# Kernel tuning notes

Measured on AMD Instinct MI355X. Metric: run time of the kernel, lower is better.

The kernel has to match this reference:

```python
import jax, jax.numpy as jnp
import numpy as np

# Poincare ball, curvature c = 1.0 (manifold.c)
C = 1.0
SQC = 1.0  # sqrt(C)
EPS = 1e-15
BALL_EPS = 1e-5
ALPHA = 0.1  # params[0]


def _project(x):
    # clip points back inside the open ball
    norm = jnp.linalg.norm(x, axis=-1, keepdims=True)
    maxnorm = (1.0 - BALL_EPS) / SQC
    return jnp.where(norm > maxnorm, x / jnp.maximum(norm, EPS) * maxnorm, x)


def _artanh(x):
    return jnp.arctanh(jnp.clip(x, -1.0 + 1e-7, 1.0 - 1e-7))


def _lambda_x(x):
    # conformal factor lambda_x = 2 / (1 - c||x||^2)
    return 2.0 / jnp.maximum(1.0 - C * jnp.sum(x * x, axis=-1, keepdims=True), EPS)


def _mobius_scalar_mul(r, x):
    n = jnp.maximum(jnp.linalg.norm(x, axis=-1, keepdims=True), EPS)
    return jnp.tanh(r * _artanh(SQC * n)) * x / (SQC * n)


def _mobius_add(x, y):
    x2 = jnp.sum(x * x, axis=-1, keepdims=True)
    y2 = jnp.sum(y * y, axis=-1, keepdims=True)
    xy = jnp.sum(x * y, axis=-1, keepdims=True)
    num = (1.0 + 2.0 * C * xy + C * y2) * x + (1.0 - C * x2) * y
    den = 1.0 + 2.0 * C * xy + C * C * x2 * y2
    return num / jnp.maximum(den, EPS)


def _expmap0(u):
    n = jnp.maximum(jnp.linalg.norm(u, axis=-1, keepdims=True), EPS)
    return jnp.tanh(SQC * n) * u / (SQC * n)


def _mobius_matvec(W, x):
    # Mobius matrix-vector multiply: expmap0-style rescale of x @ W^T
    xn = jnp.maximum(jnp.linalg.norm(x, axis=-1, keepdims=True), EPS)
    mx = x @ W.T
    mxn = jnp.maximum(jnp.linalg.norm(mx, axis=-1, keepdims=True), EPS)
    res = jnp.tanh(mxn / xn * _artanh(SQC * xn)) * mx / (SQC * mxn)
    return _project(res)


def _clamp_abs(x, eps=1e-10):
    return jnp.where(x >= 0, jnp.maximum(x, eps), jnp.minimum(x, -eps))


def weighted_midpoint_spmm(x, src, dst, w, n):
    # gyro-midpoint of neighbors under sparse adjacency weights
    gamma = _lambda_x(x)                                   # [N,1]
    msg = (gamma * x)[src] * w[:, None]                    # [E,d] irregular gather
    num = jax.ops.segment_sum(msg, dst, num_segments=n)    # [N,d]
    den = jax.ops.segment_sum(jnp.abs(w) * (gamma[:, 0] - 1.0)[src], dst,
                              num_segments=n)[:, None]     # [N,1]
    return _project(_mobius_scalar_mul(0.5, num / _clamp_abs(den)))


def weighted_midpoint_pair(a, b, wa, wb):
    # weighted_midpoint(stack([a,b],dim=1), weights=[wa,wb], reducedim=[1])
    ga, gb = _lambda_x(a), _lambda_x(b)
    num = wa * ga * a + wb * gb * b
    den = abs(wa) * (ga - 1.0) + abs(wb) * (gb - 1.0)
    return _project(_mobius_scalar_mul(0.5, num / _clamp_abs(den)))


def setup_inputs() -> dict:
    key = jax.random.key(0)
    kx, kh, kw, kW, kb, ks, kd = jax.random.split(key, 7)
    N, D, E = 100000, 48, 1600000

    def to_ball(u):
        # squash gaussian samples well inside the Poincare ball
        n = jnp.linalg.norm(u, axis=-1, keepdims=True)
        return 0.5 * u / (1.0 + n)

    x = to_ball(jax.random.normal(kx, (N, D), dtype=jnp.float32))
    h_init = to_ball(jax.random.normal(kh, (N, D), dtype=jnp.float32))
    edge_w = jax.random.uniform(kw, (E,), dtype=jnp.float32, minval=0.01, maxval=1.0)
    W = jax.random.normal(kW, (D, D), dtype=jnp.float32) * (1.0 / np.sqrt(D))
    bias = jax.random.normal(kb, (D,), dtype=jnp.float32) * 0.01
    edge_src = jax.random.randint(ks, (E,), 0, N, dtype=jnp.int32)
    edge_dst = jax.random.randint(kd, (E,), 0, N, dtype=jnp.int32)
    return {"x": x, "h_init": h_init, "edge_w": edge_w, "W": W, "bias": bias,
            "edge_src": edge_src, "edge_dst": edge_dst}


def reference(x, h_init, edge_w, W, bias, edge_src, edge_dst):
    n = x.shape[0]
    # 1) sparse adjacency-weighted hyperbolic midpoint aggregation
    support = weighted_midpoint_spmm(x, edge_src, edge_dst, edge_w, n)
    # 2) residual midpoint with h_init, weights [1-alpha, alpha]
    support = weighted_midpoint_pair(support, h_init, 1.0 - ALPHA, ALPHA)
    # 3) Mobius linear (HyperbolicLinearFast, eval-mode dropout, no nonlin)
    h = _mobius_matvec(W, support)
    h = _project(_mobius_add(h, _expmap0(bias[None, :])))
    return h
```

## Files before the change

kernel.cpp:

```cpp
#include <hip/hip_runtime.h>
#include <math.h>

#define D  48
#define DQ 12
#define SPAN 128
#define SHIFT 7
#define PCH  8192
#define PTH  512

constexpr float F_EPS   = 1e-15f;
constexpr float MAXNORM = 1.0f - 1e-5f;

__device__ __forceinline__ float artanh_c(float x) {
    x = fminf(x, 1.0f - 1e-7f);
    x = fmaxf(x, -1.0f + 1e-7f);
    return atanhf(x);
}

__device__ __forceinline__ float clampabs(float x) {
    return (x >= 0.0f) ? fmaxf(x, 1e-10f) : fminf(x, -1e-10f);
}

__device__ __forceinline__ unsigned short f2bf(float f) {
    unsigned u = __float_as_uint(f);
    u += 0x7FFFu + ((u >> 16) & 1u);
    return (unsigned short)(u >> 16);
}

__device__ __forceinline__ float bf2f(unsigned short u) {
    return __uint_as_float(((unsigned)u) << 16);
}

__global__ void k_gamma(const float* __restrict__ x, float* __restrict__ gam,
                        int* __restrict__ ghist, int n, int nb)
{
    int i = blockIdx.x * blockDim.x + threadIdx.x;
    if (i < nb) ghist[i] = 0;
    if (i >= n) return;
    const float4* xr = reinterpret_cast<const float4*>(x) + (size_t)i * DQ;
    float s = 0.0f;
#pragma unroll
    for (int q = 0; q < DQ; ++q) {
        float4 v = xr[q];
        s += v.x * v.x + v.y * v.y + v.z * v.z + v.w * v.w;
    }
    gam[i] = 2.0f / fmaxf(1.0f - s, F_EPS);
}

__global__ __launch_bounds__(PTH) void k_hist(const int* __restrict__ dst,
                                              int* __restrict__ ghist, int E, int nb)
{
    __shared__ int h[1024];
    int t = threadIdx.x;
    for (int i = t; i < 1024; i += PTH) h[i] = 0;
    __syncthreads();
    int base = blockIdx.x * PCH;
#pragma unroll 4
    for (int k = 0; k < PCH / PTH; ++k) {
        int i = base + k * PTH + t;
        if (i < E) {
            unsigned b = ((unsigned)dst[i]) >> SHIFT;
            if (b < 1024u) atomicAdd(&h[b], 1);
        }
    }
    __syncthreads();
    for (int i = t; i < nb; i += PTH) {
        int c = h[i];
        if (c) atomicAdd(&ghist[i], c);
    }
}

__global__ __launch_bounds__(1024) void k_scanb(const int* __restrict__ ghist,
                                                int* __restrict__ gstart,
                                                int* __restrict__ gcur, int nb, int E)
{
    __shared__ int sh[1024];
    int t = threadIdx.x;
    int v = (t < nb) ? ghist[t] : 0;
    sh[t] = v;
    __syncthreads();
    for (int off = 1; off < 1024; off <<= 1) {
        int a = sh[t];
        int b = (t >= off) ? sh[t - off] : 0;
        __syncthreads();
        sh[t] = a + b;
        __syncthreads();
    }
    if (t < nb) { int s = sh[t] - v; gstart[t] = s; gcur[t] = s; }
    if (t == 0) gstart[nb] = E;
}

__global__ __launch_bounds__(PTH) void k_part(const int* __restrict__ src,
                                              const int* __restrict__ dst,
                                              const float* __restrict__ w,
                                              const float* __restrict__ gam,
                                              int* __restrict__ gcur,
                                              int2* __restrict__ seg, int E, int nb)
{
    __shared__ int hist[1024];
    __shared__ int base_[1024];
    __shared__ int lcur[1024];
    int t = threadIdx.x;
    for (int i = t; i < 1024; i += PTH) { hist[i] = 0; base_[i] = 0; lcur[i] = 0; }
    __syncthreads();
    int b0 = blockIdx.x * PCH;
#pragma unroll 4
    for (int k = 0; k < PCH / PTH; ++k) {
        int i = b0 + k * PTH + t;
        if (i < E) {
            unsigned b = ((unsigned)dst[i]) >> SHIFT;
            if (b < 1024u) atomicAdd(&hist[b], 1);
        }
    }
    __syncthreads();
    for (int i = t; i < nb; i += PTH) {
        int c = hist[i];
        if (c) base_[i] = atomicAdd(&gcur[i], c);
    }
    __syncthreads();
#pragma unroll 4
    for (int k = 0; k < PCH / PTH; ++k) {
        int i = b0 + k * PTH + t;
        if (i < E) {
            int d = dst[i];
            unsigned b = ((unsigned)d) >> SHIFT;
            if (b < 1024u) {
                int s = src[i];
                float wv = w[i];
                float g  = gam[s];
                unsigned short wb  = f2bf(wv);
                unsigned short wdb = f2bf(fabsf(wv) * (g - 1.0f));
                int pos = base_[b] + atomicAdd(&lcur[b], 1);
                if (pos >= 0 && pos < E) {
                    int2 r;
                    r.x = ((d & (SPAN - 1)) << 24) | (s & 0xFFFFFF);
                    r.y = ((unsigned)wb << 16) | wdb;
                    seg[pos] = r;
                }
            }
        }
    }
}

__global__ __launch_bounds__(256) void k_sortb(
    const int2* __restrict__ seg, const int* __restrict__ gstart,
    int* __restrict__ starts, int2* __restrict__ seg2, int n, int E)
{
    __shared__ int hist[SPAN];
    __shared__ int sb[SPAN];
    __shared__ int cur[SPAN];
    int b = blockIdx.x;
    int t = threadIdx.x;
    if (b == 0 && t == 0) starts[n] = E;
    int segL = gstart[b], segR = gstart[b + 1];
    if (segL < 0) segL = 0;
    if (segR > E) segR = E;
    if (t < SPAN) hist[t] = 0;
    __syncthreads();
    {
        int j = segL + t;
        for (; j + 768 < segR; j += 1024) {
            unsigned d0 = ((unsigned)seg[j      ].x) >> 24;
            unsigned d1 = ((unsigned)seg[j + 256].x) >> 24;
            unsigned d2 = ((unsigned)seg[j + 512].x) >> 24;
            unsigned d3 = ((unsigned)seg[j + 768].x) >> 24;
            atomicAdd(&hist[d0], 1);
            atomicAdd(&hist[d1], 1);
            atomicAdd(&hist[d2], 1);
            atomicAdd(&hist[d3], 1);
        }
        for (; j < segR; j += 256) {
            unsigned dl = ((unsigned)seg[j].x) >> 24;
            atomicAdd(&hist[dl], 1);
        }
    }
    __syncthreads();
    if (t < SPAN) sb[t] = hist[t];
    __syncthreads();
    for (int off = 1; off < SPAN; off <<= 1) {
        int a = 0;
        if (t < SPAN) { a = sb[t]; if (t >= off) a += sb[t - off]; }
        __syncthreads();
        if (t < SPAN) sb[t] = a;
        __syncthreads();
    }
    if (t < SPAN) {
        int ls = sb[t] - hist[t];
        cur[t] = segL + ls;
        int node = b * SPAN + t;
        if (node < n) starts[node] = segL + ls;
    }
    __syncthreads();
    {
        int j = segL + t;
        for (; j + 768 < segR; j += 1024) {
            int2 r0 = seg[j      ];
            int2 r1 = seg[j + 256];
            int2 r2 = seg[j + 512];
            int2 r3 = seg[j + 768];
            int p0 = atomicAdd(&cur[((unsigned)r0.x) >> 24], 1);
            int p1 = atomicAdd(&cur[((unsigned)r1.x) >> 24], 1);
            int p2 = atomicAdd(&cur[((unsigned)r2.x) >> 24], 1);
            int p3 = atomicAdd(&cur[((unsigned)r3.x) >> 24], 1);
            if (p0 >= 0 && p0 < E) seg2[p0] = make_int2(r0.x & 0xFFFFFF, r0.y);
            if (p1 >= 0 && p1 < E) seg2[p1] = make_int2(r1.x & 0xFFFFFF, r1.y);
            if (p2 >= 0 && p2 < E) seg2[p2] = make_int2(r2.x & 0xFFFFFF, r2.y);
            if (p3 >= 0 && p3 < E) seg2[p3] = make_int2(r3.x & 0xFFFFFF, r3.y);
        }
        for (; j < segR; j += 256) {
            int2 r = seg[j];
            int pos = atomicAdd(&cur[((unsigned)r.x) >> 24], 1);
            if (pos >= 0 && pos < E) seg2[pos] = make_int2(r.x & 0xFFFFFF, r.y);
        }
    }
}

__global__ __launch_bounds__(256) void k_prep(const float* __restrict__ x,
                                              const float* __restrict__ gam,
                                              ushort4* __restrict__ ybf, int n)
{
    long long t = (long long)blockIdx.x * blockDim.x + threadIdx.x;
    int node = (int)(t / DQ);
    if (node >= n) return;
    int part = (int)(t % DQ);
    float g = gam[node];
    float4 v = reinterpret_cast<const float4*>(x)[(size_t)node * DQ + part];
    ushort4 o;
    o.x = f2bf(v.x * g);
    o.y = f2bf(v.y * g);
    o.z = f2bf(v.z * g);
    o.w = f2bf(v.w * g);
    ybf[(size_t)node * DQ + part] = o;
}

__global__ __launch_bounds__(256) void k_gather(
    const ushort4* __restrict__ ybf,
    const int* __restrict__ starts,
    const int2* __restrict__ srec,
    float* __restrict__ num, float* __restrict__ den, int n, int E)
{
    long long t = (long long)blockIdx.x * blockDim.x + threadIdx.x;
    int node = (int)(t / DQ);
    if (node >= n) return;
    int part = (int)(t % DQ);
    int j0 = starts[node], j1 = starts[node + 1];
    if (j0 < 0) j0 = 0;
    if (j1 > E) j1 = E;
    float4 acc = make_float4(0.f, 0.f, 0.f, 0.f);
    float dacc = 0.f;
    int j = j0;
    for (; j + 3 < j1; j += 4) {
        int2 r0 = srec[j];
        int2 r1 = srec[j + 1];
        int2 r2 = srec[j + 2];
        int2 r3 = srec[j + 3];
        ushort4 a0 = ybf[(size_t)(r0.x) * DQ + part];
        ushort4 a1 = ybf[(size_t)(r1.x) * DQ + part];
        ushort4 a2 = ybf[(size_t)(r2.x) * DQ + part];
        ushort4 a3 = ybf[(size_t)(r3.x) * DQ + part];
        float w0 = bf2f((unsigned short)(((unsigned)r0.y) >> 16));
        float w1 = bf2f((unsigned short)(((unsigned)r1.y) >> 16));
        float w2 = bf2f((unsigned short)(((unsigned)r2.y) >> 16));
        float w3 = bf2f((unsigned short)(((unsigned)r3.y) >> 16));
        acc.x = fmaf(w0, bf2f(a0.x), acc.x);
        acc.y = fmaf(w0, bf2f(a0.y), acc.y);
        acc.z = fmaf(w0, bf2f(a0.z), acc.z);
        acc.w = fmaf(w0, bf2f(a0.w), acc.w);
        acc.x = fmaf(w1, bf2f(a1.x), acc.x);
        acc.y = fmaf(w1, bf2f(a1.y), acc.y);
        acc.z = fmaf(w1, bf2f(a1.z), acc.z);
        acc.w = fmaf(w1, bf2f(a1.w), acc.w);
        acc.x = fmaf(w2, bf2f(a2.x), acc.x);
        acc.y = fmaf(w2, bf2f(a2.y), acc.y);
        acc.z = fmaf(w2, bf2f(a2.z), acc.z);
        acc.w = fmaf(w2, bf2f(a2.w), acc.w);
        acc.x = fmaf(w3, bf2f(a3.x), acc.x);
        acc.y = fmaf(w3, bf2f(a3.y), acc.y);
        acc.z = fmaf(w3, bf2f(a3.z), acc.z);
        acc.w = fmaf(w3, bf2f(a3.w), acc.w);
        dacc += bf2f((unsigned short)(((unsigned)r0.y) & 0xFFFF))
              + bf2f((unsigned short)(((unsigned)r1.y) & 0xFFFF))
              + bf2f((unsigned short)(((unsigned)r2.y) & 0xFFFF))
              + bf2f((unsigned short)(((unsigned)r3.y) & 0xFFFF));
    }
    for (; j < j1; ++j) {
        int2 r0 = srec[j];
        ushort4 a0 = ybf[(size_t)(r0.x) * DQ + part];
        float w0 = bf2f((unsigned short)(((unsigned)r0.y) >> 16));
        acc.x = fmaf(w0, bf2f(a0.x), acc.x);
        acc.y = fmaf(w0, bf2f(a0.y), acc.y);
        acc.z = fmaf(w0, bf2f(a0.z), acc.z);
        acc.w = fmaf(w0, bf2f(a0.w), acc.w);
        dacc += bf2f((unsigned short)(((unsigned)r0.y) & 0xFFFF));
    }
    reinterpret_cast<float4*>(num)[(size_t)node * DQ + part] = acc;
    if (part == 0) den[node] = dacc;
}

__global__ void k_init_atomic(float* __restrict__ den, float* __restrict__ num, int n)
{
    int i = blockIdx.x * blockDim.x + threadIdx.x;
    if (i >= n) return;
    den[i] = 0.0f;
    float4* nr = reinterpret_cast<float4*>(num) + (size_t)i * DQ;
    float4 z = make_float4(0.f, 0.f, 0.f, 0.f);
#pragma unroll
    for (int q = 0; q < DQ; ++q) nr[q] = z;
}

__global__ void k_edge_atomic(const float* __restrict__ x, const float* __restrict__ gam,
                              const int* __restrict__ src, const int* __restrict__ dst,
                              const float* __restrict__ w,
                              float* __restrict__ num, float* __restrict__ den, int E)
{
    long long t = (long long)blockIdx.x * blockDim.x + threadIdx.x;
    int e = (int)(t / DQ);
    if (e >= E) return;
    int part = (int)(t % DQ);
    int s = src[e];
    int d = dst[e];
    float we = w[e];
    float g  = gam[s];
    float4 xv = reinterpret_cast<const float4*>(x)[(size_t)s * DQ + part];
    float c = we * g;
    float* np_ = num + (size_t)d * D + part * 4;
    atomicAdd(np_ + 0, c * xv.x);
    atomicAdd(np_ + 1, c * xv.y);
    atomicAdd(np_ + 2, c * xv.z);
    atomicAdd(np_ + 3, c * xv.w);
    if (part == 0) atomicAdd(den + d, fabsf(we) * (g - 1.0f));
}

__device__ __forceinline__ void half_mul_project(float* v)
{
    float s = 0.f;
#pragma unroll
    for (int k = 0; k < D; ++k) s += v[k] * v[k];
    float nrm = sqrtf(s);
    float ncl = fmaxf(nrm, F_EPS);
    float t   = tanhf(0.5f * artanh_c(ncl));
    float sc  = t / ncl;
    float rn  = nrm * sc;
    if (rn > MAXNORM) sc *= MAXNORM / fmaxf(rn, F_EPS);
#pragma unroll
    for (int k = 0; k < D; ++k) v[k] *= sc;
}

__global__ __launch_bounds__(256) void k_node(
    float* __restrict__ out,
    const float* __restrict__ den,
    const float* __restrict__ h_init,
    const float* __restrict__ Wm,
    const float* __restrict__ bias, int n)
{
    __shared__ float Ws[D * D];
    __shared__ float bs[D];
    for (int k = threadIdx.x; k < D * D; k += blockDim.x) Ws[k] = Wm[k];
    if (threadIdx.x < D) bs[threadIdx.x] = bias[threadIdx.x];
    __syncthreads();

    int i = blockIdx.x * blockDim.x + threadIdx.x;
    if (i >= n) return;

    float a[D];
    {
        const float4* nr = reinterpret_cast<const float4*>(out) + (size_t)i * DQ;
        float dinv = 1.0f / clampabs(den[i]);
#pragma unroll
        for (int q = 0; q < DQ; ++q) {
            float4 v = nr[q];
            a[q * 4 + 0] = v.x * dinv;
            a[q * 4 + 1] = v.y * dinv;
            a[q * 4 + 2] = v.z * dinv;
            a[q * 4 + 3] = v.w * dinv;
        }
    }
    half_mul_project(a);

    {
        float b[D];
        const float4* hr = reinterpret_cast<const float4*>(h_init) + (size_t)i * DQ;
#pragma unroll
        for (int q = 0; q < DQ; ++q) {
            float4 v = hr[q];
            b[q * 4 + 0] = v.x; b[q * 4 + 1] = v.y;
            b[q * 4 + 2] = v.z; b[q * 4 + 3] = v.w;
        }
        float sa = 0.f, sb = 0.f;
#pragma unroll
        for (int k = 0; k < D; ++k) { sa += a[k] * a[k]; sb += b[k] * b[k]; }
        float ga = 2.0f / fmaxf(1.0f - sa, F_EPS);
        float gb = 2.0f / fmaxf(1.0f - sb, F_EPS);
        const float wa = 0.9f, wb = 0.1f;
        float dinv = 1.0f / clampabs(wa * (ga - 1.0f) + wb * (gb - 1.0f));
        float ca = wa * ga * dinv, cb = wb * gb * dinv;
#pragma unroll
        for (int k = 0; k < D; ++k) a[k] = ca * a[k] + cb * b[k];
        half_mul_project(a);
    }

    float mx[D];
    {
        float sa2 = 0.f;
#pragma unroll
        for (int k = 0; k < D; ++k) sa2 += a[k] * a[k];
        float xn = fmaxf(sqrtf(sa2), F_EPS);
        float smx = 0.f;
        for (int j = 0; j < D; ++j) {
            float acc = 0.f;
#pragma unroll
            for (int k = 0; k < D; ++k) acc = fmaf(Ws[j * D + k], a[k], acc);
            mx[j] = acc;
            smx += acc * acc;
        }
        float mxnr = sqrtf(smx);
        float mxn = fmaxf(mxnr, F_EPS);
        float tt = tanhf((mxn / xn) * artanh_c(xn));
        float sc = tt / mxn;
        float rn = mxnr * sc;
        if (rn > MAXNORM) sc *= MAXNORM / fmaxf(rn, F_EPS);
#pragma unroll
        for (int j = 0; j < D; ++j) mx[j] *= sc;
    }

    {
        float bn2 = 0.f;
#pragma unroll
        for (int k = 0; k < D; ++k) bn2 += bs[k] * bs[k];
        float bn  = fmaxf(sqrtf(bn2), F_EPS);
        float tb  = tanhf(bn);
        float ebs = tb / bn;
        float y2  = ebs * ebs * bn2;

        float x2 = 0.f, xy = 0.f;
#pragma unroll
        for (int k = 0; k < D; ++k) { x2 += mx[k] * mx[k]; xy += mx[k] * bs[k]; }
        xy *= ebs;

        float c1 = 1.0f + 2.0f * xy + y2;
        float c2 = 1.0f - x2;
        float dn3 = 1.0f / fmaxf(1.0f + 2.0f * xy + x2 * y2, F_EPS);

        float r[D];
        float s3 = 0.f;
#pragma unroll
        for (int k = 0; k < D; ++k) {
            float rv = (c1 * mx[k] + c2 * ebs * bs[k]) * dn3;
            r[k] = rv;
            s3 += rv * rv;
        }
        float nrm3 = sqrtf(s3);
        float fp = 1.0f;
        if (nrm3 > MAXNORM) fp = MAXNORM / fmaxf(nrm3, F_EPS);

        float4* orow = reinterpret_cast<float4*>(out) + (size_t)i * DQ;
#pragma unroll
        for (int q = 0; q < DQ; ++q) {
            float4 v;
            v.x = r[q * 4 + 0] * fp;
            v.y = r[q * 4 + 1] * fp;
            v.z = r[q * 4 + 2] * fp;
            v.w = r[q * 4 + 3] * fp;
            orow[q] = v;
        }
    }
}

extern "C" void kernel_launch(void* const* d_in, const int* in_sizes, int n_in,
                              void* d_out, int out_size, void* d_ws, size_t ws_size,
                              hipStream_t stream)
{
    const float* x      = (const float*)d_in[0];
    const float* h_init = (const float*)d_in[1];
    const float* edge_w = (const float*)d_in[2];
    const float* W      = (const float*)d_in[3];
    const float* bias   = (const float*)d_in[4];
    const int*   esrc   = (const int*)d_in[5];
    const int*   edst   = (const int*)d_in[6];
    float* out = (float*)d_out;

    int n = in_sizes[0] / D;
    int E = in_sizes[2];
    int nb = (n + SPAN - 1) >> SHIFT;

    char* p = (char*)d_ws;
    float* gam    = (float*)p;             p += (size_t)n * 4;
    float* den    = (float*)p;             p += (size_t)n * 4;
    int*   ghist  = (int*)p;               p += (size_t)nb * 4;
    int*   gstart = (int*)p;               p += (size_t)(nb + 1) * 4;
    int*   gcur   = (int*)p;               p += (size_t)nb * 4;
    int*   starts = (int*)p;               p += (size_t)(n + 1) * 4;
    p = (char*)(((uintptr_t)p + 15) & ~(uintptr_t)15);
    int2*  seg    = (int2*)p;              p += (size_t)E * 8;
    int2*  seg2   = (int2*)p;              p += (size_t)E * 8;
    size_t need1 = (size_t)(p - (char*)d_ws);
    ushort4* ybf = (ushort4*)seg;
    bool ybf_fits = ((size_t)E * 8 >= (size_t)n * D * 2);

    k_gamma<<<(n + 255) / 256, 256, 0, stream>>>(x, gam, ghist, n, nb);

    bool shape_ok = (nb <= 1024) && (n < (1 << 24));
    if (shape_ok && ybf_fits && need1 <= ws_size) {
        int pb = (E + PCH - 1) / PCH;
        k_hist<<<pb, PTH, 0, stream>>>(edst, ghist, E, nb);
        k_scanb<<<1, 1024, 0, stream>>>(ghist, gstart, gcur, nb, E);
        k_part<<<pb, PTH, 0, stream>>>(esrc, edst, edge_w, gam, gcur, seg, E, nb);
        k_sortb<<<nb, 256, 0, stream>>>(seg, gstart, starts, seg2, n, E);
        long long tot = (long long)n * DQ;
        int gg = (int)((tot + 255) / 256);
        k_prep<<<gg, 256, 0, stream>>>(x, gam, ybf, n);
        k_gather<<<gg, 256, 0, stream>>>(ybf, starts, seg2, out, den, n, E);
    } else {
        k_init_atomic<<<(n + 255) / 256, 256, 0, stream>>>(den, out, n);
        long long tot = (long long)E * DQ;
        k_edge_atomic<<<(int)((tot + 255) / 256), 256, 0, stream>>>(x, gam, esrc, edst, edge_w, out, den, E);
    }

    k_node<<<(n + 255) / 256, 256, 0, stream>>>(out, den, h_init, W, bias, n);
}
```

Before: 148.7 us.

## Recompute matvec instead of storing mx, read W from global, fold norms algebraically

The node kernel no longer stages W and bias in shared memory and reads them straight from global memory, relying on uniform, cache-friendly loads. The mx[48] and r[48] register arrays are gone. The Mobius-add norms are derived in closed form from ||mx||², mx·bias and ||bias||², and the matvec is computed a second time to write the output. This cuts register pressure to raise occupancy, at the cost of doubling the 48x48 matvec FLOPs per node.

```diff
diff --git a/kernel.cpp b/kernel.cpp
--- a/kernel.cpp
+++ b/kernel.cpp
@@ -353,12 +353,6 @@
     const float* __restrict__ Wm,
     const float* __restrict__ bias, int n)
 {
-    __shared__ float Ws[D * D];
-    __shared__ float bs[D];
-    for (int k = threadIdx.x; k < D * D; k += blockDim.x) Ws[k] = Wm[k];
-    if (threadIdx.x < D) bs[threadIdx.x] = bias[threadIdx.x];
-    __syncthreads();
-
     int i = blockIdx.x * blockDim.x + threadIdx.x;
     if (i >= n) return;
 
@@ -399,70 +393,63 @@
         half_mul_project(a);
     }
 
-    float mx[D];
-    {
-        float sa2 = 0.f;
-#pragma unroll
-        for (int k = 0; k < D; ++k) sa2 += a[k] * a[k];
-        float xn = fmaxf(sqrtf(sa2), F_EPS);
-        float smx = 0.f;
-        for (int j = 0; j < D; ++j) {
+    float sa2 = 0.f;
+#pragma unroll
+    for (int k = 0; k < D; ++k) sa2 += a[k] * a[k];
+    float xn = fmaxf(sqrtf(sa2), F_EPS);
+
+    float smx = 0.f, xyr = 0.f;
+#pragma unroll 4
+    for (int j = 0; j < D; ++j) {
+        float acc = 0.f;
+#pragma unroll
+        for (int k = 0; k < D; ++k) acc = fmaf(Wm[j * D + k], a[k], acc);
+        smx += acc * acc;
+        xyr = fmaf(acc, bias[j], xyr);
+    }
+    float mxnr = sqrtf(smx);
+    float mxn = fmaxf(mxnr, F_EPS);
+    float tt = tanhf((mxn / xn) * artanh_c(xn));
+    float sc = tt / mxn;
+    float rn = mxnr * sc;
+    if (rn > MAXNORM) sc *= MAXNORM / fmaxf(rn, F_EPS);
+
+    float bn2 = 0.f;
+#pragma unroll
+    for (int k = 0; k < D; ++k) bn2 = fmaf(bias[k], bias[k], bn2);
+    float bn  = fmaxf(sqrtf(bn2), F_EPS);
+    float ebs = tanhf(bn) / bn;
+    float y2  = ebs * ebs * bn2;
+
+    float x2 = sc * sc * smx;
+    float xy = sc * ebs * xyr;
+    float c1 = 1.0f + 2.0f * xy + y2;
+    float c2 = 1.0f - x2;
+    float dn3 = 1.0f / fmaxf(1.0f + 2.0f * xy + x2 * y2, F_EPS);
+
+    float s3 = dn3 * dn3 * (c1 * c1 * sc * sc * smx
+                            + 2.0f * c1 * c2 * sc * ebs * xyr
+                            + c2 * c2 * ebs * ebs * bn2);
+    float nrm3 = sqrtf(s3);
+    float fp = (nrm3 > MAXNORM) ? (MAXNORM / fmaxf(nrm3, F_EPS)) : 1.0f;
+
+    float CA = c1 * sc * dn3 * fp;
+    float CB = c2 * ebs * dn3 * fp;
+
+    float4* orow = reinterpret_cast<float4*>(out) + (size_t)i * DQ;
+    for (int q = 0; q < DQ; ++q) {
+        float e[4];
+#pragma unroll
+        for (int jj = 0; jj < 4; ++jj) {
+            int j = q * 4 + jj;
             float acc = 0.f;
 #pragma unroll
-            for (int k = 0; k < D; ++k) acc = fmaf(Ws[j * D + k], a[k], acc);
-            mx[j] = acc;
-            smx += acc * acc;
-        }
-        float mxnr = sqrtf(smx);
-        float mxn = fmaxf(mxnr, F_EPS);
-        float tt = tanhf((mxn / xn) * artanh_c(xn));
-        float sc = tt / mxn;
-        float rn = mxnr * sc;
-        if (rn > MAXNORM) sc *= MAXNORM / fmaxf(rn, F_EPS);
-#pragma unroll
-        for (int j = 0; j < D; ++j) mx[j] *= sc;
-    }
-
-    {
-        float bn2 = 0.f;
-#pragma unroll
-        for (int k = 0; k < D; ++k) bn2 += bs[k] * bs[k];
-        float bn  = fmaxf(sqrtf(bn2), F_EPS);
-        float tb  = tanhf(bn);
-        float ebs = tb / bn;
-        float y2  = ebs * ebs * bn2;
-
-        float x2 = 0.f, xy = 0.f;
-#pragma unroll
-        for (int k = 0; k < D; ++k) { x2 += mx[k] * mx[k]; xy += mx[k] * bs[k]; }
-        xy *= ebs;
-
-        float c1 = 1.0f + 2.0f * xy + y2;
-        float c2 = 1.0f - x2;
-        float dn3 = 1.0f / fmaxf(1.0f + 2.0f * xy + x2 * y2, F_EPS);
-
-        float r[D];
-        float s3 = 0.f;
-#pragma unroll
-        for (int k = 0; k < D; ++k) {
-            float rv = (c1 * mx[k] + c2 * ebs * bs[k]) * dn3;
-            r[k] = rv;
-            s3 += rv * rv;
-        }
-        float nrm3 = sqrtf(s3);
-        float fp = 1.0f;
-        if (nrm3 > MAXNORM) fp = MAXNORM / fmaxf(nrm3, F_EPS);
-
-        float4* orow = reinterpret_cast<float4*>(out) + (size_t)i * DQ;
-#pragma unroll
-        for (int q = 0; q < DQ; ++q) {
-            float4 v;
-            v.x = r[q * 4 + 0] * fp;
-            v.y = r[q * 4 + 1] * fp;
-            v.z = r[q * 4 + 2] * fp;
-            v.w = r[q * 4 + 3] * fp;
-            orow[q] = v;
-        }
+            for (int k = 0; k < D; ++k) acc = fmaf(Wm[j * D + k], a[k], acc);
+            e[jj] = fmaf(CA, acc, CB * bias[j]);
+        }
+        float4 v;
+        v.x = e[0]; v.y = e[1]; v.z = e[2]; v.w = e[3];
+        orow[q] = v;
     }
 }
 
```

Result: slower. 164.3 us (+10.5%).
